# Performance work log

Measured on AMD Instinct MI355X. Metric: run time of the kernel, lower is better.

The kernel has to match this reference:

```python
import jax, jax.numpy as jnp
import numpy as np

B, N, D = 32, 8192, 256

def setup_inputs() -> dict:
    key = jax.random.key(0)
    kx, km, kq = jax.random.split(key, 3)
    x = jax.random.normal(kx, (B, N, D), dtype=jnp.float32)
    mask = jax.random.randint(km, (B, N), 0, 2) > 0
    # ensure at least one valid position per row so softmax is well-defined
    mask = mask.at[:, 0].set(True)
    q = jax.random.normal(kq, (D,), dtype=jnp.float32)
    return {"x": x, "mask": mask, "q": q}

def reference(x, mask, q) -> jnp.ndarray:
    # logits: [B, N]
    logits = jnp.einsum('bnd,d->bn', x, q)
    logits = jnp.where(mask, logits, -jnp.inf)
    w = jax.nn.softmax(logits, axis=-1)  # [B, N]
    return jnp.einsum('bn,bnd->bd', w, x)  # [B, D]
```

## Files before the change

### kernel.cpp

```cpp
#include <hip/hip_runtime.h>
#include <math.h>


#define BB 32
#define NN 8192
#define DD 256
#define CHUNKS 32
#define ROWS_PER_CHUNK (NN / CHUNKS)
#define ROWS_PER_WAVE 64

__global__ __launch_bounds__(256) void pool_partial(
    const float* __restrict__ x,
    const int*   __restrict__ mask,
    const float* __restrict__ q,
    float* __restrict__ acc_part,
    float* __restrict__ m_part,
    float* __restrict__ s_part)
{
    const int b     = blockIdx.x / CHUNKS;
    const int chunk = blockIdx.x % CHUNKS;
    const int wave  = threadIdx.x >> 6;
    const int lane  = threadIdx.x & 63;

    const int row0 = chunk * ROWS_PER_CHUNK + wave * ROWS_PER_WAVE;

    const float4 qv = reinterpret_cast<const float4*>(q)[lane];

    const int mv = mask[(size_t)b * NN + row0 + lane];
    unsigned long long act = __ballot(mv != 0);

    float  m = -INFINITY, s = 0.0f;
    float4 acc = make_float4(0.f, 0.f, 0.f, 0.f);

    const float4* xb = reinterpret_cast<const float4*>(x + (size_t)b * NN * DD);

    while (act) {
        const int j = __ffsll((long long)act) - 1;
        act &= act - 1;
        const int row = row0 + j;

        const float4 xv = xb[(size_t)row * (DD / 4) + lane];

        float part = xv.x * qv.x + xv.y * qv.y + xv.z * qv.z + xv.w * qv.w;
        #pragma unroll
        for (int off = 32; off > 0; off >>= 1)
            part += __shfl_xor(part, off, 64);
        const float logit = part;

        if (logit > m) {
            const float sc = __expf(m - logit);
            s = s * sc + 1.0f;
            acc.x = acc.x * sc + xv.x;
            acc.y = acc.y * sc + xv.y;
            acc.z = acc.z * sc + xv.z;
            acc.w = acc.w * sc + xv.w;
            m = logit;
        } else {
            const float p = __expf(logit - m);
            s += p;
            acc.x += p * xv.x;
            acc.y += p * xv.y;
            acc.z += p * xv.z;
            acc.w += p * xv.w;
        }
    }

    __shared__ float lacc[4][DD];
    __shared__ float lm[4], ls[4];
    reinterpret_cast<float4*>(lacc[wave])[lane] = acc;
    if (lane == 0) { lm[wave] = m; ls[wave] = s; }
    __syncthreads();

    const int t = threadIdx.x;
    const float mstar = fmaxf(fmaxf(lm[0], lm[1]), fmaxf(lm[2], lm[3]));
    float stot = 0.f, a = 0.f;
    #pragma unroll
    for (int w = 0; w < 4; ++w) {
        const float wgt = (ls[w] > 0.f) ? __expf(lm[w] - mstar) : 0.f;
        stot += wgt * ls[w];
        a    += wgt * lacc[w][t];
    }
    const int pi = b * CHUNKS + chunk;
    acc_part[(size_t)pi * DD + t] = a;
    if (t == 0) { m_part[pi] = mstar; s_part[pi] = stot; }
}

__global__ __launch_bounds__(256) void pool_final(
    const float* __restrict__ acc_part,
    const float* __restrict__ m_part,
    const float* __restrict__ s_part,
    float* __restrict__ out)
{
    const int b = blockIdx.x;
    const int t = threadIdx.x;

    __shared__ float sm[CHUNKS], ss[CHUNKS];
    if (t < CHUNKS) {
        sm[t] = m_part[b * CHUNKS + t];
        ss[t] = s_part[b * CHUNKS + t];
    }
    __syncthreads();

    float M = -INFINITY;
    #pragma unroll
    for (int c = 0; c < CHUNKS; ++c)
        if (ss[c] > 0.f) M = fmaxf(M, sm[c]);

    float S = 0.f, a = 0.f;
    #pragma unroll
    for (int c = 0; c < CHUNKS; ++c) {
        const float wgt = (ss[c] > 0.f) ? __expf(sm[c] - M) : 0.f;
        S += wgt * ss[c];
        a += wgt * acc_part[((size_t)b * CHUNKS + c) * DD + t];
    }
    out[b * DD + t] = a / S;
}

extern "C" void kernel_launch(void* const* d_in, const int* in_sizes, int n_in,
                              void* d_out, int out_size, void* d_ws, size_t ws_size,
                              hipStream_t stream) {
    const float* x    = (const float*)d_in[0];
    const int*   mask = (const int*)  d_in[1];
    const float* q    = (const float*)d_in[2];
    float* out = (float*)d_out;

    float* acc_part = (float*)d_ws;
    float* m_part   = acc_part + (size_t)BB * CHUNKS * DD;
    float* s_part   = m_part + (size_t)BB * CHUNKS;

    pool_partial<<<BB * CHUNKS, 256, 0, stream>>>(x, mask, q, acc_part, m_part, s_part);
    pool_final<<<BB, 256, 0, stream>>>(acc_part, m_part, s_part, out);
}
```

Baseline: 338.3 us.

## Split each wave into four row groups with software-prefetched loads

Measured after the change: 337.3 us. Within noise of the previous version (-0.3%).

```diff
diff --git a/kernel.cpp b/kernel.cpp
--- a/kernel.cpp
+++ b/kernel.cpp
@@ -6,8 +6,17 @@
 #define NN 8192
 #define DD 256
 #define CHUNKS 32
-#define ROWS_PER_CHUNK (NN / CHUNKS)
-#define ROWS_PER_WAVE 64
+#define RPC (NN / CHUNKS)
+
+__device__ __forceinline__ float dot4(float4 a, float4 b) {
+    return fmaf(a.x, b.x, fmaf(a.y, b.y, fmaf(a.z, b.z, a.w * b.w)));
+}
+
+#define UPD(A, C)                       \
+    A.x = fmaf(A.x, sc, w * C.x);       \
+    A.y = fmaf(A.y, sc, w * C.y);       \
+    A.z = fmaf(A.z, sc, w * C.z);       \
+    A.w = fmaf(A.w, sc, w * C.w);
 
 __global__ __launch_bounds__(256) void pool_partial(
     const float* __restrict__ x,
@@ -21,68 +30,74 @@
     const int chunk = blockIdx.x % CHUNKS;
     const int wave  = threadIdx.x >> 6;
     const int lane  = threadIdx.x & 63;
+    const int g     = lane >> 4;
+    const int c     = lane & 15;
 
-    const int row0 = chunk * ROWS_PER_CHUNK + wave * ROWS_PER_WAVE;
+    const int row0 = chunk * RPC + wave * 64;
 
-    const float4 qv = reinterpret_cast<const float4*>(q)[lane];
+    const float4* q4 = reinterpret_cast<const float4*>(q) + c * 4;
+    const float4 q0 = q4[0], q1 = q4[1], q2 = q4[2], q3 = q4[3];
 
     const int mv = mask[(size_t)b * NN + row0 + lane];
-    unsigned long long act = __ballot(mv != 0);
+    const unsigned long long wmask = __ballot(mv != 0);
+    unsigned long long qm = wmask & (0x1111111111111111ULL << g);
 
-    float  m = -INFINITY, s = 0.0f;
-    float4 acc = make_float4(0.f, 0.f, 0.f, 0.f);
+    float m = -INFINITY, s = 0.0f;
+    float4 a0 = make_float4(0.f, 0.f, 0.f, 0.f), a1 = a0, a2 = a0, a3 = a0;
 
     const float4* xb = reinterpret_cast<const float4*>(x + (size_t)b * NN * DD);
 
-    while (act) {
-        const int j = __ffsll((long long)act) - 1;
-        act &= act - 1;
-        const int row = row0 + j;
-
-        const float4 xv = xb[(size_t)row * (DD / 4) + lane];
-
-        float part = xv.x * qv.x + xv.y * qv.y + xv.z * qv.z + xv.w * qv.w;
-        #pragma unroll
-        for (int off = 32; off > 0; off >>= 1)
-            part += __shfl_xor(part, off, 64);
-        const float logit = part;
-
-        if (logit > m) {
-            const float sc = __expf(m - logit);
-            s = s * sc + 1.0f;
-            acc.x = acc.x * sc + xv.x;
-            acc.y = acc.y * sc + xv.y;
-            acc.z = acc.z * sc + xv.z;
-            acc.w = acc.w * sc + xv.w;
-            m = logit;
-        } else {
-            const float p = __expf(logit - m);
-            s += p;
-            acc.x += p * xv.x;
-            acc.y += p * xv.y;
-            acc.z += p * xv.z;
-            acc.w += p * xv.w;
+    if (qm) {
+        int j = __ffsll(qm) - 1; qm &= qm - 1;
+        const float4* rp = xb + (size_t)(row0 + j) * (DD / 4) + c * 4;
+        float4 c0 = rp[0], c1 = rp[1], c2 = rp[2], c3 = rp[3];
+        for (;;) {
+            const bool more = (qm != 0ULL);
+            float4 n0 = a0, n1 = a0, n2 = a0, n3 = a0;
+            if (more) {
+                const int jn = __ffsll(qm) - 1; qm &= qm - 1;
+                const float4* np = xb + (size_t)(row0 + jn) * (DD / 4) + c * 4;
+                n0 = np[0]; n1 = np[1]; n2 = np[2]; n3 = np[3];
+            }
+            float p = dot4(c0, q0) + dot4(c1, q1) + dot4(c2, q2) + dot4(c3, q3);
+            p += __shfl_xor(p, 1, 16);
+            p += __shfl_xor(p, 2, 16);
+            p += __shfl_xor(p, 4, 16);
+            p += __shfl_xor(p, 8, 16);
+            const float mnew = fmaxf(m, p);
+            const float sc = __expf(m - mnew);
+            const float w  = __expf(p - mnew);
+            s = fmaf(s, sc, w);
+            UPD(a0, c0); UPD(a1, c1); UPD(a2, c2); UPD(a3, c3);
+            m = mnew;
+            if (!more) break;
+            c0 = n0; c1 = n1; c2 = n2; c3 = n3;
         }
     }
 
-    __shared__ float lacc[4][DD];
-    __shared__ float lm[4], ls[4];
-    reinterpret_cast<float4*>(lacc[wave])[lane] = acc;
-    if (lane == 0) { lm[wave] = m; ls[wave] = s; }
+    __shared__ float lacc[16][DD];
+    __shared__ float lm[16], ls[16];
+    const int sid = wave * 4 + g;
+    float4* dst = reinterpret_cast<float4*>(&lacc[sid][c * 16]);
+    dst[0] = a0; dst[1] = a1; dst[2] = a2; dst[3] = a3;
+    if (c == 0) { lm[sid] = m; ls[sid] = s; }
     __syncthreads();
 
     const int t = threadIdx.x;
-    const float mstar = fmaxf(fmaxf(lm[0], lm[1]), fmaxf(lm[2], lm[3]));
-    float stot = 0.f, a = 0.f;
+    float M = -INFINITY;
     #pragma unroll
-    for (int w = 0; w < 4; ++w) {
-        const float wgt = (ls[w] > 0.f) ? __expf(lm[w] - mstar) : 0.f;
-        stot += wgt * ls[w];
-        a    += wgt * lacc[w][t];
+    for (int i = 0; i < 16; ++i)
+        if (ls[i] > 0.f) M = fmaxf(M, lm[i]);
+    float S = 0.f, A = 0.f;
+    #pragma unroll
+    for (int i = 0; i < 16; ++i) {
+        const float wgt = (ls[i] > 0.f) ? __expf(lm[i] - M) : 0.f;
+        S += wgt * ls[i];
+        A += wgt * lacc[i][t];
     }
     const int pi = b * CHUNKS + chunk;
-    acc_part[(size_t)pi * DD + t] = a;
-    if (t == 0) { m_part[pi] = mstar; s_part[pi] = stot; }
+    acc_part[(size_t)pi * DD + t] = A;
+    if (t == 0) { m_part[pi] = M; s_part[pi] = S; }
 }
 
 __global__ __launch_bounds__(256) void pool_final(
```
